# Kernel tuning notes

Measured on AMD Instinct MI355X. Metric: run time of the kernel, lower is better.

## Reference

```python
import jax, jax.numpy as jnp
import numpy as np

EPS = 1e-12


def setup_inputs() -> dict:
    key = jax.random.key(0)
    x = jax.random.normal(key, (32, 3000, 512), dtype=jnp.float32)
    return {"x": x, "kernel_size": 100}


def _window_sum(a, k):
    # sliding sum of length-k windows (stride 1) along axis 1; a: [B, Tpad, D] -> [B, Tpad-k+1, D]
    return jax.lax.reduce_window(a, 0.0, jax.lax.add, (1, k, 1), (1, 1, 1), 'VALID')


def reference(x, kernel_size):
    k = int(kernel_size)
    B, T, D = x.shape
    if T < k:
        # global CMVN fallback (torch.std default is unbiased, ddof=1)
        m = x.mean(axis=1, keepdims=True)
        v = x.std(axis=1, ddof=1, keepdims=True)
        return (x - m) / (v + EPS)
    # per-position effective window counts matching torch's denom construction:
    # ramp k//2..k-1, then k for the interior, then k-1 down to k//2
    denom = jnp.concatenate([
        jnp.arange(k // 2, k),
        jnp.full((T - k,), k),
        jnp.arange(k - 1, k // 2 - 1, -1),
    ]).astype(x.dtype)[None, :, None]  # [1, T, 1]
    # zero-pad time axis exactly like F.pad(..., (k//2, k//2 - 1))
    x_pad = jnp.pad(x, ((0, 0), (k // 2, k // 2 - 1), (0, 0)))
    s1 = _window_sum(x_pad, k)            # sum of window values (zeros at pads) [B, T, D]
    s2 = _window_sum(x_pad * x_pad, k)    # sum of squares                        [B, T, D]
    m = s1 / denom
    # torch sums (window - m)^2 over all k slots INCLUDING zero-padded slots:
    # sum (w - m)^2 = s2 - 2*m*s1 + k*m^2
    var_sum = s2 - 2.0 * m * s1 + k * m * m
    v = jnp.sqrt(var_sum / (k - 1))
    return (x - m) / (v + EPS)
```

## Files before the change

### kernel.cpp

```cpp
#include <hip/hip_runtime.h>

#define EPS 1e-12f


typedef float f4 __attribute__((ext_vector_type(4)));

constexpr int Bq = 32, Tq = 3000, Dq = 512;
constexpr int SEGR = 25;
constexpr int NSEG = Tq / SEGR;
constexpr int WT = 4;
constexpr int TB = SEGR * WT;
constexpr int NGRP = Tq / TB;
constexpr int NBm = Bq * NGRP;
constexpr int NXCD = 8;

__global__ __launch_bounds__(128) void seg_sums_kernel(
    const float* __restrict__ x, float* __restrict__ ws)
{
    const int s = blockIdx.x;
    const int b = blockIdx.y;
    const int d4 = threadIdx.x;
    const float* xp = x + ((size_t)b * Tq) * Dq + (size_t)d4 * 4;

    f4 a1 = {0.f, 0.f, 0.f, 0.f};
    f4 a2 = a1, b1 = a1, b2 = a1;
    const int r0 = s * SEGR;
#pragma unroll 5
    for (int j = 0; j < SEGR; j += 2) {
        const f4 v = *(const f4*)(xp + (size_t)(r0 + j) * Dq);
        a1 += v; a2 += v * v;
        if (j + 1 < SEGR) {
            const f4 w = *(const f4*)(xp + (size_t)(r0 + j + 1) * Dq);
            b1 += w; b2 += w * w;
        }
    }
    f4* w1 = (f4*)ws;
    f4* w2 = w1 + (size_t)Bq * NSEG * (Dq / 4);
    const size_t idx = ((size_t)b * NSEG + s) * (Dq / 4) + d4;
    w1[idx] = a1 + b1;
    w2[idx] = a2 + b2;
}

__global__ __launch_bounds__(512, 8) void mavn_kernel(
    const float* __restrict__ x, const int* __restrict__ kptr,
    float* __restrict__ out, const float* __restrict__ ws, int use_seg)
{
    const int g = blockIdx.x;
    const int xcd = g & (NXCD - 1);
    const int slot = g >> 3;
    const int pair = xcd * (NBm / NXCD) + slot;
    const int b = pair / NGRP;
    const int grp = pair % NGRP;

    const int tid = threadIdx.x;
    const int w = tid >> 6;
    const int l = tid & 63;
    const int q = w >> 1;
    const int dh = w & 1;

    const int c = grp * WT + q;
    const int t0 = c * SEGR;
    const int t1 = t0 + SEGR;

    const int k = kptr[0];
    const int half = k >> 1;
    const size_t bbase = (size_t)b * Tq * Dq;
    const int doff = dh * (Dq / 2) + l * 4;
    const float* xp = x + bbase + doff;
    float* op = out + bbase + doff;

    const float kf = (float)k;
    const float inv_km1 = 1.0f / (float)(k - 1);
    const int tail_start = Tq - (k - half);

    const bool seg_ok = use_seg && (k == 4 * SEGR);
    const bool interior = seg_ok && (t0 >= half) &&
                          (t0 + SEGR - 1 + (k - half) - 1 <= Tq - 1) &&
                          (t0 + SEGR - 1 < tail_start);

    if (interior) {
        const f4* w1 = (const f4*)ws;
        const f4* w2 = w1 + (size_t)Bq * NSEG * (Dq / 4);
        const int colf4 = dh * (Dq / 8) + l;
        f4 s1 = {0.f, 0.f, 0.f, 0.f};
        f4 s2 = s1;
#pragma unroll
        for (int i = 0; i < 4; ++i) {
            const size_t idx = ((size_t)b * NSEG + (c - 2 + i)) * (Dq / 4) + colf4;
            s1 += w1[idx];
            s2 += w2[idx];
        }
        const float inv_k = 1.0f / kf;
        {
            const f4 xc = *(const f4*)(xp + (size_t)t0 * Dq);
            f4 o;
#pragma unroll
            for (int cc = 0; cc < 4; ++cc) {
                const float m = s1[cc] * inv_k;
                float var_sum = s2[cc] - m * s1[cc];
                var_sum = fmaxf(var_sum, 1e-12f);
                const float r = __builtin_amdgcn_rsqf(var_sum * inv_km1);
                o[cc] = (xc[cc] - m) * r;
            }
            __builtin_nontemporal_store(o, (f4*)(op + (size_t)t0 * Dq));
        }
        const int inoff = (k - half) - 1;
        const int oboff = -(half + 1);
        f4 n0 = *(const f4*)(xp + (size_t)(t0 + 1) * Dq);
        f4 n1 = *(const f4*)(xp + (size_t)(t0 + 2) * Dq);
        f4 i0 = *(const f4*)(xp + (size_t)(t0 + 1 + inoff) * Dq);
        f4 i1 = *(const f4*)(xp + (size_t)(t0 + 2 + inoff) * Dq);
        f4 o0 = *(const f4*)(xp + (size_t)(t0 + 1 + oboff) * Dq);
        f4 o1 = *(const f4*)(xp + (size_t)(t0 + 2 + oboff) * Dq);
        for (int j = 1; j < SEGR; j += 2) {
            const f4 cn0 = n0, cn1 = n1, ci0 = i0, ci1 = i1, co0 = o0, co1 = o1;
            {
                const int jn = (j + 2 <= SEGR - 2) ? j + 2 : j;
                n0 = *(const f4*)(xp + (size_t)(t0 + jn) * Dq);
                n1 = *(const f4*)(xp + (size_t)(t0 + jn + 1) * Dq);
                i0 = *(const f4*)(xp + (size_t)(t0 + jn + inoff) * Dq);
                i1 = *(const f4*)(xp + (size_t)(t0 + jn + 1 + inoff) * Dq);
                o0 = *(const f4*)(xp + (size_t)(t0 + jn + oboff) * Dq);
                o1 = *(const f4*)(xp + (size_t)(t0 + jn + 1 + oboff) * Dq);
            }
            s1 += ci0 - co0;
            s2 += ci0 * ci0 - co0 * co0;
            f4 oa;
#pragma unroll
            for (int cc = 0; cc < 4; ++cc) {
                const float m = s1[cc] * inv_k;
                float var_sum = s2[cc] - m * s1[cc];
                var_sum = fmaxf(var_sum, 1e-12f);
                const float r = __builtin_amdgcn_rsqf(var_sum * inv_km1);
                oa[cc] = (cn0[cc] - m) * r;
            }
            __builtin_nontemporal_store(oa, (f4*)(op + (size_t)(t0 + j) * Dq));
            s1 += ci1 - co1;
            s2 += ci1 * ci1 - co1 * co1;
            f4 ob2;
#pragma unroll
            for (int cc = 0; cc < 4; ++cc) {
                const float m = s1[cc] * inv_k;
                float var_sum = s2[cc] - m * s1[cc];
                var_sum = fmaxf(var_sum, 1e-12f);
                const float r = __builtin_amdgcn_rsqf(var_sum * inv_km1);
                ob2[cc] = (cn1[cc] - m) * r;
            }
            __builtin_nontemporal_store(ob2, (f4*)(op + (size_t)(t0 + j + 1) * Dq));
        }
        return;
    }

    f4 s1 = {0.f, 0.f, 0.f, 0.f};
    f4 s2 = s1;
    {
        const int wlo = (t0 - half > 0) ? t0 - half : 0;
        const int whi = (t0 + (k - half) < Tq) ? t0 + (k - half) : Tq;
        f4 a1 = s1, a2 = s1;
        int j = wlo;
        for (; j + 1 < whi; j += 2) {
            const f4 v = *(const f4*)(xp + (size_t)j * Dq);
            const f4 u = *(const f4*)(xp + (size_t)(j + 1) * Dq);
            s1 += v; s2 += v * v;
            a1 += u; a2 += u * u;
        }
        if (j < whi) {
            const f4 v = *(const f4*)(xp + (size_t)j * Dq);
            s1 += v; s2 += v * v;
        }
        s1 += a1; s2 += a2;
    }

    f4 nx = *(const f4*)(xp + (size_t)t0 * Dq);
    f4 ia = {0.f, 0.f, 0.f, 0.f};
    f4 ob = ia;
    float wa = 0.f, wb = 0.f;

    for (int t = t0; t < t1; ++t) {
        const f4 cnum = nx;
        const f4 cin = ia;
        const f4 cout = ob;
        const float cwa = wa, cwb = wb;

        {
            const int tn = (t + 1 < t1) ? t + 1 : t;
            nx = *(const f4*)(xp + (size_t)tn * Dq);
            int ja = tn + (k - half) - 1;
            int jr = tn - half - 1;
            wa = (ja < Tq && tn > t0) ? 1.f : 0.f;
            wb = (jr >= 0 && tn > t0) ? 1.f : 0.f;
            ja = ja < Tq - 1 ? ja : Tq - 1; ja = ja > 0 ? ja : 0;
            jr = jr > 0 ? jr : 0;
            ia = *(const f4*)(xp + (size_t)ja * Dq);
            ob = *(const f4*)(xp + (size_t)jr * Dq);
        }

        s1 += cwa * cin - cwb * cout;
        s2 += cwa * cin * cin - cwb * cout * cout;

        int idn = half + t;
        idn = idn < k ? idn : k;
        const int tail = (k - 1) - (t - tail_start);
        idn = idn < tail ? idn : tail;
        const float inv_denom = __builtin_amdgcn_rcpf((float)idn);

        f4 o;
#pragma unroll
        for (int cc = 0; cc < 4; ++cc) {
            const float m = s1[cc] * inv_denom;
            float var_sum = s2[cc] - 2.0f * m * s1[cc] + kf * m * m;
            var_sum = fmaxf(var_sum, 0.0f);
            const float sd = __builtin_amdgcn_sqrtf(var_sum * inv_km1);
            o[cc] = (cnum[cc] - m) * __builtin_amdgcn_rcpf(sd + EPS);
        }
        __builtin_nontemporal_store(o, (f4*)(op + (size_t)t * Dq));
    }
}

extern "C" void kernel_launch(void* const* d_in, const int* in_sizes, int n_in,
                              void* d_out, int out_size, void* d_ws, size_t ws_size,
                              hipStream_t stream) {
    const float* x = (const float*)d_in[0];
    const int* kptr = (const int*)d_in[1];
    float* out = (float*)d_out;
    (void)in_sizes; (void)n_in; (void)out_size;

    const size_t ws_need = 2ull * Bq * NSEG * Dq * sizeof(float);
    const int use_seg = (d_ws != nullptr && ws_size >= ws_need) ? 1 : 0;

    if (use_seg) {
        dim3 g1(NSEG, Bq);
        seg_sums_kernel<<<g1, 128, 0, stream>>>(x, (float*)d_ws);
    }
    mavn_kernel<<<NBm, 512, 0, stream>>>(x, kptr, out, (const float*)d_ws, use_seg);
}
```

Before: 123.2 us.

## Stage interior window loads through an LDS double-buffer ring with async global-to-LDS copies

```diff
diff --git a/kernel.cpp b/kernel.cpp
--- a/kernel.cpp
+++ b/kernel.cpp
@@ -8,11 +8,15 @@
 constexpr int Bq = 32, Tq = 3000, Dq = 512;
 constexpr int SEGR = 25;
 constexpr int NSEG = Tq / SEGR;
-constexpr int WT = 4;
-constexpr int TB = SEGR * WT;
-constexpr int NGRP = Tq / TB;
-constexpr int NBm = Bq * NGRP;
+constexpr int NCHUNK = Tq / SEGR;
+constexpr int NBm = Bq * NCHUNK;
 constexpr int NXCD = 8;
+
+__device__ __forceinline__ void gl_lds16(const float* g, float* l) {
+    __builtin_amdgcn_global_load_lds(
+        (const __attribute__((address_space(1))) void*)g,
+        (__attribute__((address_space(3))) void*)l, 16, 0, 0);
+}
 
 __global__ __launch_bounds__(128) void seg_sums_kernel(
     const float* __restrict__ x, float* __restrict__ ws)
@@ -41,33 +45,29 @@
     w2[idx] = a2 + b2;
 }
 
-__global__ __launch_bounds__(512, 8) void mavn_kernel(
+__global__ __launch_bounds__(128, 2) void mavn_kernel(
     const float* __restrict__ x, const int* __restrict__ kptr,
     float* __restrict__ out, const float* __restrict__ ws, int use_seg)
 {
+    __shared__ float ring[2][2][3][3][256];
+
     const int g = blockIdx.x;
     const int xcd = g & (NXCD - 1);
     const int slot = g >> 3;
     const int pair = xcd * (NBm / NXCD) + slot;
-    const int b = pair / NGRP;
-    const int grp = pair % NGRP;
-
+    const int b = pair / NCHUNK;
+    const int c = pair % NCHUNK;
+    const int t0 = c * SEGR;
+    const int t1 = t0 + SEGR;
+
+    const int k = kptr[0];
+    const int half = k >> 1;
     const int tid = threadIdx.x;
     const int w = tid >> 6;
-    const int l = tid & 63;
-    const int q = w >> 1;
-    const int dh = w & 1;
-
-    const int c = grp * WT + q;
-    const int t0 = c * SEGR;
-    const int t1 = t0 + SEGR;
-
-    const int k = kptr[0];
-    const int half = k >> 1;
-    const size_t bbase = (size_t)b * Tq * Dq;
-    const int doff = dh * (Dq / 2) + l * 4;
-    const float* xp = x + bbase + doff;
-    float* op = out + bbase + doff;
+    const int l4 = (tid & 63) * 4;
+    const size_t base = ((size_t)b * Tq) * (size_t)Dq + (size_t)tid * 4;
+    const float* xp = x + base;
+    float* op = out + base;
 
     const float kf = (float)k;
     const float inv_km1 = 1.0f / (float)(k - 1);
@@ -81,12 +81,11 @@
     if (interior) {
         const f4* w1 = (const f4*)ws;
         const f4* w2 = w1 + (size_t)Bq * NSEG * (Dq / 4);
-        const int colf4 = dh * (Dq / 8) + l;
         f4 s1 = {0.f, 0.f, 0.f, 0.f};
         f4 s2 = s1;
 #pragma unroll
         for (int i = 0; i < 4; ++i) {
-            const size_t idx = ((size_t)b * NSEG + (c - 2 + i)) * (Dq / 4) + colf4;
+            const size_t idx = ((size_t)b * NSEG + (c - 2 + i)) * (Dq / 4) + tid;
             s1 += w1[idx];
             s2 += w2[idx];
         }
@@ -104,49 +103,58 @@
             }
             __builtin_nontemporal_store(o, (f4*)(op + (size_t)t0 * Dq));
         }
+
         const int inoff = (k - half) - 1;
         const int oboff = -(half + 1);
-        f4 n0 = *(const f4*)(xp + (size_t)(t0 + 1) * Dq);
-        f4 n1 = *(const f4*)(xp + (size_t)(t0 + 2) * Dq);
-        f4 i0 = *(const f4*)(xp + (size_t)(t0 + 1 + inoff) * Dq);
-        f4 i1 = *(const f4*)(xp + (size_t)(t0 + 2 + inoff) * Dq);
-        f4 o0 = *(const f4*)(xp + (size_t)(t0 + 1 + oboff) * Dq);
-        f4 o1 = *(const f4*)(xp + (size_t)(t0 + 2 + oboff) * Dq);
-        for (int j = 1; j < SEGR; j += 2) {
-            const f4 cn0 = n0, cn1 = n1, ci0 = i0, ci1 = i1, co0 = o0, co1 = o1;
-            {
-                const int jn = (j + 2 <= SEGR - 2) ? j + 2 : j;
-                n0 = *(const f4*)(xp + (size_t)(t0 + jn) * Dq);
-                n1 = *(const f4*)(xp + (size_t)(t0 + jn + 1) * Dq);
-                i0 = *(const f4*)(xp + (size_t)(t0 + jn + inoff) * Dq);
-                i1 = *(const f4*)(xp + (size_t)(t0 + jn + 1 + inoff) * Dq);
-                o0 = *(const f4*)(xp + (size_t)(t0 + jn + oboff) * Dq);
-                o1 = *(const f4*)(xp + (size_t)(t0 + jn + 1 + oboff) * Dq);
+
+        auto stage = [&](int buf, int grp) {
+#pragma unroll
+            for (int r = 0; r < 3; ++r) {
+                int j = 1 + 3 * grp + r;
+                j = (j <= SEGR - 1) ? j : SEGR - 1;
+                const float* pn = xp + (size_t)(t0 + j) * Dq;
+                const float* pi = xp + (size_t)(t0 + j + inoff) * Dq;
+                const float* po = xp + (size_t)(t0 + j + oboff) * Dq;
+                gl_lds16(pn, &ring[w][buf][r][0][0]);
+                gl_lds16(pi, &ring[w][buf][r][1][0]);
+                gl_lds16(po, &ring[w][buf][r][2][0]);
             }
-            s1 += ci0 - co0;
-            s2 += ci0 * ci0 - co0 * co0;
-            f4 oa;
-#pragma unroll
-            for (int cc = 0; cc < 4; ++cc) {
-                const float m = s1[cc] * inv_k;
-                float var_sum = s2[cc] - m * s1[cc];
-                var_sum = fmaxf(var_sum, 1e-12f);
-                const float r = __builtin_amdgcn_rsqf(var_sum * inv_km1);
-                oa[cc] = (cn0[cc] - m) * r;
+        };
+        auto compute = [&](int buf, int grp) {
+#pragma unroll
+            for (int r = 0; r < 3; ++r) {
+                const int j = 1 + 3 * grp + r;
+                const f4 cn = *(const f4*)&ring[w][buf][r][0][l4];
+                const f4 ci = *(const f4*)&ring[w][buf][r][1][l4];
+                const f4 co = *(const f4*)&ring[w][buf][r][2][l4];
+                s1 += ci - co;
+                s2 += ci * ci - co * co;
+                f4 o;
+#pragma unroll
+                for (int cc = 0; cc < 4; ++cc) {
+                    const float m = s1[cc] * inv_k;
+                    float var_sum = s2[cc] - m * s1[cc];
+                    var_sum = fmaxf(var_sum, 1e-12f);
+                    const float r2 = __builtin_amdgcn_rsqf(var_sum * inv_km1);
+                    o[cc] = (cn[cc] - m) * r2;
+                }
+                __builtin_nontemporal_store(o, (f4*)(op + (size_t)(t0 + j) * Dq));
             }
-            __builtin_nontemporal_store(oa, (f4*)(op + (size_t)(t0 + j) * Dq));
-            s1 += ci1 - co1;
-            s2 += ci1 * ci1 - co1 * co1;
-            f4 ob2;
-#pragma unroll
-            for (int cc = 0; cc < 4; ++cc) {
-                const float m = s1[cc] * inv_k;
-                float var_sum = s2[cc] - m * s1[cc];
-                var_sum = fmaxf(var_sum, 1e-12f);
-                const float r = __builtin_amdgcn_rsqf(var_sum * inv_km1);
-                ob2[cc] = (cn1[cc] - m) * r;
-            }
-            __builtin_nontemporal_store(ob2, (f4*)(op + (size_t)(t0 + j + 1) * Dq));
+        };
+
+        stage(0, 0);
+        stage(1, 1);
+        asm volatile("s_waitcnt vmcnt(9)" ::: "memory");
+        __builtin_amdgcn_sched_barrier(0);
+        compute(0, 0);
+        asm volatile("" ::: "memory");
+#pragma unroll
+        for (int gg = 1; gg < 8; ++gg) {
+            stage((gg + 1) & 1, gg + 1);
+            asm volatile("s_waitcnt vmcnt(12)" ::: "memory");
+            __builtin_amdgcn_sched_barrier(0);
+            compute(gg & 1, gg);
+            asm volatile("" ::: "memory");
         }
         return;
     }
@@ -232,5 +240,5 @@
         dim3 g1(NSEG, Bq);
         seg_sums_kernel<<<g1, 128, 0, stream>>>(x, (float*)d_ws);
     }
-    mavn_kernel<<<NBm, 512, 0, stream>>>(x, kptr, out, (const float*)d_ws, use_seg);
-}
+    mavn_kernel<<<NBm, 128, 0, stream>>>(x, kptr, out, (const float*)d_ws, use_seg);
+}
```

Result: faster. 106.4 us (-13.6%).

## Use one 128-thread block per segment and unroll the interior loop three-way

Applied to the files above, without the earlier changes.

```diff
diff --git a/kernel.cpp b/kernel.cpp
--- a/kernel.cpp
+++ b/kernel.cpp
@@ -8,10 +8,8 @@
 constexpr int Bq = 32, Tq = 3000, Dq = 512;
 constexpr int SEGR = 25;
 constexpr int NSEG = Tq / SEGR;
-constexpr int WT = 4;
-constexpr int TB = SEGR * WT;
-constexpr int NGRP = Tq / TB;
-constexpr int NBm = Bq * NGRP;
+constexpr int NCHUNK = Tq / SEGR;
+constexpr int NBm = Bq * NCHUNK;
 constexpr int NXCD = 8;
 
 __global__ __launch_bounds__(128) void seg_sums_kernel(
@@ -41,7 +39,7 @@
     w2[idx] = a2 + b2;
 }
 
-__global__ __launch_bounds__(512, 8) void mavn_kernel(
+__global__ __launch_bounds__(128) void mavn_kernel(
     const float* __restrict__ x, const int* __restrict__ kptr,
     float* __restrict__ out, const float* __restrict__ ws, int use_seg)
 {
@@ -49,25 +47,17 @@
     const int xcd = g & (NXCD - 1);
     const int slot = g >> 3;
     const int pair = xcd * (NBm / NXCD) + slot;
-    const int b = pair / NGRP;
-    const int grp = pair % NGRP;
-
-    const int tid = threadIdx.x;
-    const int w = tid >> 6;
-    const int l = tid & 63;
-    const int q = w >> 1;
-    const int dh = w & 1;
-
-    const int c = grp * WT + q;
+    const int b = pair / NCHUNK;
+    const int c = pair % NCHUNK;
     const int t0 = c * SEGR;
     const int t1 = t0 + SEGR;
 
     const int k = kptr[0];
     const int half = k >> 1;
-    const size_t bbase = (size_t)b * Tq * Dq;
-    const int doff = dh * (Dq / 2) + l * 4;
-    const float* xp = x + bbase + doff;
-    float* op = out + bbase + doff;
+    const int d4 = threadIdx.x;
+    const size_t base = ((size_t)b * Tq) * (size_t)Dq + (size_t)d4 * 4;
+    const float* xp = x + base;
+    float* op = out + base;
 
     const float kf = (float)k;
     const float inv_km1 = 1.0f / (float)(k - 1);
@@ -81,12 +71,11 @@
     if (interior) {
         const f4* w1 = (const f4*)ws;
         const f4* w2 = w1 + (size_t)Bq * NSEG * (Dq / 4);
-        const int colf4 = dh * (Dq / 8) + l;
         f4 s1 = {0.f, 0.f, 0.f, 0.f};
         f4 s2 = s1;
 #pragma unroll
         for (int i = 0; i < 4; ++i) {
-            const size_t idx = ((size_t)b * NSEG + (c - 2 + i)) * (Dq / 4) + colf4;
+            const size_t idx = ((size_t)b * NSEG + (c - 2 + i)) * (Dq / 4) + d4;
             s1 += w1[idx];
             s2 += w2[idx];
         }
@@ -108,45 +97,68 @@
         const int oboff = -(half + 1);
         f4 n0 = *(const f4*)(xp + (size_t)(t0 + 1) * Dq);
         f4 n1 = *(const f4*)(xp + (size_t)(t0 + 2) * Dq);
+        f4 n2 = *(const f4*)(xp + (size_t)(t0 + 3) * Dq);
         f4 i0 = *(const f4*)(xp + (size_t)(t0 + 1 + inoff) * Dq);
         f4 i1 = *(const f4*)(xp + (size_t)(t0 + 2 + inoff) * Dq);
+        f4 i2 = *(const f4*)(xp + (size_t)(t0 + 3 + inoff) * Dq);
         f4 o0 = *(const f4*)(xp + (size_t)(t0 + 1 + oboff) * Dq);
         f4 o1 = *(const f4*)(xp + (size_t)(t0 + 2 + oboff) * Dq);
-        for (int j = 1; j < SEGR; j += 2) {
-            const f4 cn0 = n0, cn1 = n1, ci0 = i0, ci1 = i1, co0 = o0, co1 = o1;
+        f4 o2 = *(const f4*)(xp + (size_t)(t0 + 3 + oboff) * Dq);
+#pragma unroll
+        for (int gg = 0; gg < 8; ++gg) {
+            const int j0 = 1 + 3 * gg;
+            const int jn = (gg < 7) ? j0 + 3 : j0;
             {
-                const int jn = (j + 2 <= SEGR - 2) ? j + 2 : j;
+                s1 += i0 - o0;
+                s2 += i0 * i0 - o0 * o0;
+                f4 o;
+#pragma unroll
+                for (int cc = 0; cc < 4; ++cc) {
+                    const float m = s1[cc] * inv_k;
+                    float var_sum = s2[cc] - m * s1[cc];
+                    var_sum = fmaxf(var_sum, 1e-12f);
+                    const float r = __builtin_amdgcn_rsqf(var_sum * inv_km1);
+                    o[cc] = (n0[cc] - m) * r;
+                }
+                __builtin_nontemporal_store(o, (f4*)(op + (size_t)(t0 + j0) * Dq));
                 n0 = *(const f4*)(xp + (size_t)(t0 + jn) * Dq);
+                i0 = *(const f4*)(xp + (size_t)(t0 + jn + inoff) * Dq);
+                o0 = *(const f4*)(xp + (size_t)(t0 + jn + oboff) * Dq);
+            }
+            {
+                s1 += i1 - o1;
+                s2 += i1 * i1 - o1 * o1;
+                f4 o;
+#pragma unroll
+                for (int cc = 0; cc < 4; ++cc) {
+                    const float m = s1[cc] * inv_k;
+                    float var_sum = s2[cc] - m * s1[cc];
+                    var_sum = fmaxf(var_sum, 1e-12f);
+                    const float r = __builtin_amdgcn_rsqf(var_sum * inv_km1);
+                    o[cc] = (n1[cc] - m) * r;
+                }
+                __builtin_nontemporal_store(o, (f4*)(op + (size_t)(t0 + j0 + 1) * Dq));
                 n1 = *(const f4*)(xp + (size_t)(t0 + jn + 1) * Dq);
-                i0 = *(const f4*)(xp + (size_t)(t0 + jn + inoff) * Dq);
                 i1 = *(const f4*)(xp + (size_t)(t0 + jn + 1 + inoff) * Dq);
-                o0 = *(const f4*)(xp + (size_t)(t0 + jn + oboff) * Dq);
                 o1 = *(const f4*)(xp + (size_t)(t0 + jn + 1 + oboff) * Dq);
             }
-            s1 += ci0 - co0;
-            s2 += ci0 * ci0 - co0 * co0;
-            f4 oa;
-#pragma unroll
-            for (int cc = 0; cc < 4; ++cc) {
-                const float m = s1[cc] * inv_k;
-                float var_sum = s2[cc] - m * s1[cc];
-                var_sum = fmaxf(var_sum, 1e-12f);
-                const float r = __builtin_amdgcn_rsqf(var_sum * inv_km1);
-                oa[cc] = (cn0[cc] - m) * r;
-            }
-            __builtin_nontemporal_store(oa, (f4*)(op + (size_t)(t0 + j) * Dq));
-            s1 += ci1 - co1;
-            s2 += ci1 * ci1 - co1 * co1;
-            f4 ob2;
-#pragma unroll
-            for (int cc = 0; cc < 4; ++cc) {
-                const float m = s1[cc] * inv_k;
-                float var_sum = s2[cc] - m * s1[cc];
-                var_sum = fmaxf(var_sum, 1e-12f);
-                const float r = __builtin_amdgcn_rsqf(var_sum * inv_km1);
-                ob2[cc] = (cn1[cc] - m) * r;
-            }
-            __builtin_nontemporal_store(ob2, (f4*)(op + (size_t)(t0 + j + 1) * Dq));
+            {
+                s1 += i2 - o2;
+                s2 += i2 * i2 - o2 * o2;
+                f4 o;
+#pragma unroll
+                for (int cc = 0; cc < 4; ++cc) {
+                    const float m = s1[cc] * inv_k;
+                    float var_sum = s2[cc] - m * s1[cc];
+                    var_sum = fmaxf(var_sum, 1e-12f);
+                    const float r = __builtin_amdgcn_rsqf(var_sum * inv_km1);
+                    o[cc] = (n2[cc] - m) * r;
+                }
+                __builtin_nontemporal_store(o, (f4*)(op + (size_t)(t0 + j0 + 2) * Dq));
+                n2 = *(const f4*)(xp + (size_t)(t0 + jn + 2) * Dq);
+                i2 = *(const f4*)(xp + (size_t)(t0 + jn + 2 + inoff) * Dq);
+                o2 = *(const f4*)(xp + (size_t)(t0 + jn + 2 + oboff) * Dq);
+            }
         }
         return;
     }
@@ -232,5 +244,5 @@
         dim3 g1(NSEG, Bq);
         seg_sums_kernel<<<g1, 128, 0, stream>>>(x, (float*)d_ws);
     }
-    mavn_kernel<<<NBm, 512, 0, stream>>>(x, kptr, out, (const float*)d_ws, use_seg);
+    mavn_kernel<<<NBm, 128, 0, stream>>>(x, kptr, out, (const float*)d_ws, use_seg);
 }
```

New measurement: 109.2 us. 1.13x faster.
